# Performance work log

Hardware: AMD Instinct MI355X
Metric: run time of the kernel (lower is better)

The kernel has to match this reference:

```python
import jax, jax.numpy as jnp
import numpy as np

N = 2048
D_T = 256; D_F = 256
E_T = 32; E_F = 32; E_C = 128
C = 5; Q = 512


def setup_inputs() -> dict:
    key = jax.random.key(0)
    ks = jax.random.split(key, 12)
    # full graph minus self-loops, row-major (matches dense_to_sparse ordering)
    r, c = np.meshgrid(np.arange(N), np.arange(N), indexing='ij')
    m = r != c
    edge_index = jnp.asarray(np.stack([r[m], c[m]]), dtype=jnp.int32)  # [2, N*(N-1)]
    E = edge_index.shape[1]
    s = 0.02
    return {
        'time_features': jax.random.normal(ks[0], (N, D_T), jnp.float32),
        'edge_index': edge_index,
        'time_edge_weight': jax.random.uniform(ks[1], (E,), jnp.float32),
        'freq_features': jax.random.normal(ks[2], (N, D_F), jnp.float32),
        'freq_edge_weight': jax.random.uniform(ks[3], (E,), jnp.float32),
        'labels': jax.random.randint(ks[4], (N,), 0, C, jnp.int32),
        'num_classes': C,
        'query_size': Q,
        'Wt': jax.random.normal(ks[5], (D_T, E_T), jnp.float32) * s,
        'bt': jnp.zeros((E_T,), jnp.float32),
        'Wf': jax.random.normal(ks[6], (D_F, E_F), jnp.float32) * s,
        'bf': jnp.zeros((E_F,), jnp.float32),
        'Wc': jax.random.normal(ks[7], (E_T + E_F + C, E_C), jnp.float32) * s,
        'bc': jnp.zeros((E_C,), jnp.float32),
        'Wo': jax.random.normal(ks[8], (E_C, C), jnp.float32) * s,
        'bo': jnp.zeros((C,), jnp.float32),
    }


def _gcn(x, A, W, b):
    # torch_geometric GCNConv: D^{-1/2}(A + I)D^{-1/2} (X W) + b
    n = A.shape[0]
    Ah = A + jnp.eye(n, dtype=A.dtype)
    deg = Ah.sum(axis=1)
    dis = jnp.where(deg > 0, jax.lax.rsqrt(deg), 0.0)
    return (dis[:, None] * Ah * dis[None, :]) @ (x @ W) + b


def reference(time_features, edge_index, time_edge_weight, freq_features,
              freq_edge_weight, labels, num_classes, query_size,
              Wt, bt, Wf, bf, Wc, bc, Wo, bo):
    n = time_features.shape[0]
    lrelu = lambda z: jax.nn.leaky_relu(z, 0.01)

    def dense_adj(w):  # A[dst, src] = w
        return jnp.zeros((n, n), w.dtype).at[edge_index[1], edge_index[0]].add(w)

    te = lrelu(_gcn(time_features, dense_adj(time_edge_weight), Wt, bt))
    fe = lrelu(_gcn(freq_features, dense_adj(freq_edge_weight), Wf, bf))

    # to_one_hot: one_hot[:n - query_size, labels] = 1 -> support rows get 1 in
    # every column that appears anywhere in `labels`
    cols = jnp.zeros((num_classes,), te.dtype).at[labels].set(1.0)
    rowmask = (jnp.arange(n) < (n - query_size)).astype(te.dtype)
    one_hot = rowmask[:, None] * cols[None, :]

    feats = jnp.concatenate([te, fe, one_hot], axis=-1)  # [n, E_T+E_F+C]

    # graph_construction (no_grad in original): 1 / (L1 distance over the
    # non-one-hot dims + 1e-5), zero diagonal
    fd = jax.lax.stop_gradient(feats[:, : feats.shape[1] - num_classes])
    dist = jnp.sum(jnp.abs(fd[:, None, :] - fd[None, :, :]), axis=-1)  # [n, n]
    Aw = (1.0 / (dist + 1e-5)) * (1.0 - jnp.eye(n, dtype=feats.dtype))

    emb = lrelu(_gcn(feats, Aw, Wc, bc))
    return emb @ Wo + bo
```

## Files before the change

### kernel.cpp

```cpp
#include <hip/hip_runtime.h>
#include <hip/hip_bf16.h>

#define N 2048
#define NM1 2047
#define DT 256
#define ET 32
#define EC 128
#define NC 5
#define FS 80
#define FD 69
#define KC_ET 16
#define KC_EC 16

typedef unsigned short u16;
typedef float f32x4 __attribute__((ext_vector_type(4)));
typedef __bf16 bf16x8 __attribute__((ext_vector_type(8)));

__device__ inline u16 bf16_rne(float x){
    unsigned int b = __float_as_uint(x);
    b += 0x7fffu + ((b >> 16) & 1u);
    return (u16)(b >> 16);
}
__device__ inline float bf16_to_f(u16 h){
    return __uint_as_float(((unsigned int)h) << 16);
}
__device__ inline f32x4 mfma16x16x32(bf16x8 a, bf16x8 b, f32x4 c){
    return __builtin_amdgcn_mfma_f32_16x16x32_bf16(a, b, c, 0, 0, 0);
}

__global__ __launch_bounds__(256) void k_deg_label_xw(const float* __restrict__ tw,
                                                      const float* __restrict__ fw,
                                                      const int* __restrict__ labels,
                                                      const float* __restrict__ Xt,
                                                      const float* __restrict__ Wt,
                                                      const float* __restrict__ Xf,
                                                      const float* __restrict__ Wf,
                                                      float* __restrict__ degT,
                                                      float* __restrict__ degF,
                                                      float* __restrict__ cols,
                                                      float* __restrict__ Yt,
                                                      float* __restrict__ Yf){
    int b = blockIdx.x;
    int t = threadIdx.x;
    if (b < 512){
        int p = (b & 7)*256 + t;
        if (p >= NM1) return;
        int s0 = (b >> 3)*32;
        float lowT=0.f, highT=0.f, lowF=0.f, highF=0.f;
        #pragma unroll 8
        for (int r = 0; r < 32; ++r){
            int s = s0 + r;
            float vt = tw[(size_t)s*NM1 + p];
            float vf = fw[(size_t)s*NM1 + p];
            if (s <= p){ highT += vt; highF += vf; }
            else       { lowT  += vt; lowF  += vf; }
        }
        atomicAdd(&degT[p],   lowT);
        atomicAdd(&degF[p],   lowF);
        atomicAdd(&degT[p+1], highT);
        atomicAdd(&degF[p+1], highF);
        return;
    }
    if (b == 512){
        __shared__ float lc[NC];
        if (t < NC) lc[t] = 0.f;
        __syncthreads();
        for (int i = t; i < N; i += 256){
            int l = labels[i];
            if (l >= 0 && l < NC) lc[l] = 1.f;
        }
        __syncthreads();
        if (t < NC) cols[t] = lc[t];
        return;
    }
    int idx = b - 513;
    const float* X = (idx & 256) ? Xf : Xt;
    const float* W = (idx & 256) ? Wf : Wt;
    float*       Y = (idx & 256) ? Yf : Yt;
    __shared__ float Ws[DT*ET];
    __shared__ float Xs[8*DT];
    for (int j = t; j < DT*ET; j += 256) Ws[j] = W[j];
    int i0 = (idx & 255)*8;
    for (int j = t; j < 8*DT; j += 256) Xs[j] = X[(size_t)i0*DT + j];
    __syncthreads();
    int r = t >> 5, f = t & 31;
    const float* xr = Xs + r*DT;
    float acc = 0.f;
    #pragma unroll 8
    for (int d = 0; d < DT; ++d) acc += xr[d]*Ws[d*ET+f];
    Y[(size_t)(i0+r)*ET+f] = acc;
}

__global__ __launch_bounds__(256) void k_agg_et_m(const float* __restrict__ tw,
                                                  const float* __restrict__ fw,
                                                  const float* __restrict__ Yt,
                                                  const float* __restrict__ Yf,
                                                  const float* __restrict__ degT,
                                                  const float* __restrict__ degF,
                                                  float* __restrict__ Pt,
                                                  float* __restrict__ Pf){
    __shared__ u16 Zs[2][2][32][136];
    int t = threadIdx.x;
    int w = t >> 6, l = t & 63, lr = l & 15, lg = l >> 4;
    int g = w >> 1, wh = w & 1;
    int i0 = blockIdx.x*64;
    int kc = blockIdx.y;
    int k0 = kc*128;

    {
        int f = t >> 3;
        int kb16 = (t & 7)*16;
        #pragma unroll
        for (int gg = 0; gg < 2; ++gg){
            const float* Y   = gg ? Yf   : Yt;
            const float* deg = gg ? degF : degT;
            u16 h8[16], l8[16];
            #pragma unroll
            for (int j = 0; j < 16; ++j){
                int k = k0 + kb16 + j;
                float rd = rsqrtf(1.f + deg[k]);
                float v = rd * Y[(size_t)k*ET + f];
                u16 h = bf16_rne(v);
                h8[j] = h;
                l8[j] = bf16_rne(v - bf16_to_f(h));
            }
            uint4 pk;
            pk.x = (unsigned)h8[0] | ((unsigned)h8[1]<<16);
            pk.y = (unsigned)h8[2] | ((unsigned)h8[3]<<16);
            pk.z = (unsigned)h8[4] | ((unsigned)h8[5]<<16);
            pk.w = (unsigned)h8[6] | ((unsigned)h8[7]<<16);
            *(uint4*)&Zs[gg][0][f][kb16] = pk;
            pk.x = (unsigned)h8[8] | ((unsigned)h8[9]<<16);
            pk.y = (unsigned)h8[10] | ((unsigned)h8[11]<<16);
            pk.z = (unsigned)h8[12] | ((unsigned)h8[13]<<16);
            pk.w = (unsigned)h8[14] | ((unsigned)h8[15]<<16);
            *(uint4*)&Zs[gg][0][f][kb16+8] = pk;
            pk.x = (unsigned)l8[0] | ((unsigned)l8[1]<<16);
            pk.y = (unsigned)l8[2] | ((unsigned)l8[3]<<16);
            pk.z = (unsigned)l8[4] | ((unsigned)l8[5]<<16);
            pk.w = (unsigned)l8[6] | ((unsigned)l8[7]<<16);
            *(uint4*)&Zs[gg][1][f][kb16] = pk;
            pk.x = (unsigned)l8[8] | ((unsigned)l8[9]<<16);
            pk.y = (unsigned)l8[10] | ((unsigned)l8[11]<<16);
            pk.z = (unsigned)l8[12] | ((unsigned)l8[13]<<16);
            pk.w = (unsigned)l8[14] | ((unsigned)l8[15]<<16);
            *(uint4*)&Zs[gg][1][f][kb16+8] = pk;
        }
    }
    __syncthreads();

    const float* A = g ? fw : tw;
    f32x4 acc[2][2];
    #pragma unroll
    for (int fi = 0; fi < 2; ++fi)
        #pragma unroll
        for (int ff = 0; ff < 2; ++ff) acc[fi][ff] = (f32x4){0.f,0.f,0.f,0.f};

    for (int sub = 0; sub < 2; ++sub){
        int kb = k0 + sub*64;
        #pragma unroll
        for (int fi = 0; fi < 2; ++fi){
            int row = i0 + wh*32 + fi*16 + lr;
            #pragma unroll
            for (int ks = 0; ks < 2; ++ks){
                int kbase = kb + ks*32 + lg*8;
                u16 ah[8], al[8];
                #pragma unroll
                for (int j = 0; j < 8; ++j){
                    int k = kbase + j;
                    float v = 0.f;
                    if (row != k) v = A[(size_t)k*NM1 + row - (row > k ? 1 : 0)];
                    u16 h = bf16_rne(v);
                    ah[j] = h;
                    al[j] = bf16_rne(v - bf16_to_f(h));
                }
                uint4 pa, pb;
                pa.x = (unsigned)ah[0] | ((unsigned)ah[1]<<16);
                pa.y = (unsigned)ah[2] | ((unsigned)ah[3]<<16);
                pa.z = (unsigned)ah[4] | ((unsigned)ah[5]<<16);
                pa.w = (unsigned)ah[6] | ((unsigned)ah[7]<<16);
                pb.x = (unsigned)al[0] | ((unsigned)al[1]<<16);
                pb.y = (unsigned)al[2] | ((unsigned)al[3]<<16);
                pb.z = (unsigned)al[4] | ((unsigned)al[5]<<16);
                pb.w = (unsigned)al[6] | ((unsigned)al[7]<<16);
                bf16x8 aH = *(bf16x8*)&pa;
                bf16x8 aL = *(bf16x8*)&pb;
                int koff = sub*64 + ks*32 + lg*8;
                #pragma unroll
                for (int ff = 0; ff < 2; ++ff){
                    bf16x8 bH = *(const bf16x8*)&Zs[g][0][ff*16+lr][koff];
                    bf16x8 bL = *(const bf16x8*)&Zs[g][1][ff*16+lr][koff];
                    acc[fi][ff] = mfma16x16x32(aH, bH, acc[fi][ff]);
                    acc[fi][ff] = mfma16x16x32(aL, bH, acc[fi][ff]);
                    acc[fi][ff] = mfma16x16x32(aH, bL, acc[fi][ff]);
                }
            }
        }
    }
    float* P = g ? Pf : Pt;
    #pragma unroll
    for (int fi = 0; fi < 2; ++fi)
        #pragma unroll
        for (int ff = 0; ff < 2; ++ff)
            #pragma unroll
            for (int r = 0; r < 4; ++r){
                int gi = i0 + wh*32 + fi*16 + lg*4 + r;
                P[(size_t)kc*(N*ET) + (size_t)gi*ET + ff*16 + lr] = acc[fi][ff][r];
            }
}

__global__ __launch_bounds__(256) void k_feats_epi(const float* __restrict__ Pt,
                                                   const float* __restrict__ Pf,
                                                   const float* __restrict__ Yt,
                                                   const float* __restrict__ Yf,
                                                   const float* __restrict__ degT,
                                                   const float* __restrict__ degF,
                                                   const float* __restrict__ bt,
                                                   const float* __restrict__ bfv,
                                                   const float* __restrict__ cols,
                                                   const int* __restrict__ qsize,
                                                   float* __restrict__ feats){
    int idx = blockIdx.x*256 + threadIdx.x;
    int i = idx >> 6;
    int f = idx & 63;
    float s, rd, b;
    if (f < ET){
        rd = rsqrtf(1.f + degT[i]);
        s = rd*Yt[(size_t)i*ET + f];
        #pragma unroll
        for (int kc = 0; kc < KC_ET; ++kc) s += Pt[(size_t)kc*(N*ET) + (size_t)i*ET + f];
        b = bt[f];
    } else {
        int g = f - ET;
        rd = rsqrtf(1.f + degF[i]);
        s = rd*Yf[(size_t)i*ET + g];
        #pragma unroll
        for (int kc = 0; kc < KC_ET; ++kc) s += Pf[(size_t)kc*(N*ET) + (size_t)i*ET + g];
        b = bfv[g];
    }
    float v = rd*s + b;
    feats[(size_t)i*FS + f] = v > 0.f ? v : 0.01f*v;
    if (f < NC){
        int nsup = N - qsize[0];
        feats[(size_t)i*FS + 2*ET + f] = (i < nsup) ? cols[f] : 0.f;
    }
}

__global__ __launch_bounds__(256) void k_aw_zc(const float* __restrict__ feats,
                                               const float* __restrict__ Wc,
                                               u16* __restrict__ Aw_hi,
                                               u16* __restrict__ Aw_lo,
                                               u16* __restrict__ ZcT_hi,
                                               u16* __restrict__ ZcT_lo,
                                               float* __restrict__ dsum){
    __shared__ __align__(16) char sm[37632];
    int t = threadIdx.x;
    int b = blockIdx.x;
    if (b < 1024){
        float* fiT = (float*)sm;
        float* fjT = fiT + 64*68;
        int i0 = (b & 31)*64, j0 = (b >> 5)*64;
        {
            int row = t >> 2;
            int cb  = (t & 3)*16;
            const float4* si = (const float4*)(feats + (size_t)(i0+row)*FS + cb);
            const float4* sj = (const float4*)(feats + (size_t)(j0+row)*FS + cb);
            #pragma unroll
            for (int s = 0; s < 4; ++s){
                float4 v = si[s];
                float4 w = sj[s];
                int c = cb + s*4;
                fiT[(c+0)*68+row]=v.x; fiT[(c+1)*68+row]=v.y; fiT[(c+2)*68+row]=v.z; fiT[(c+3)*68+row]=v.w;
                fjT[(c+0)*68+row]=w.x; fjT[(c+1)*68+row]=w.y; fjT[(c+2)*68+row]=w.z; fjT[(c+3)*68+row]=w.w;
            }
        }
        __syncthreads();
        int tx = t & 15, ty = t >> 4;
        float acc[4][4];
        #pragma unroll
        for (int u=0;u<4;++u)
            #pragma unroll
            for (int v=0;v<4;++v) acc[u][v]=0.f;
        for (int d = 0; d < 64; ++d){
            float4 a4 = *(const float4*)&fiT[d*68 + ty*4];
            float4 b4 = *(const float4*)&fjT[d*68 + tx*4];
            const float* ap = (const float*)&a4;
            const float* bp = (const float*)&b4;
            #pragma unroll
            for (int u = 0; u < 4; ++u)
                #pragma unroll
                for (int v = 0; v < 4; ++v)
                    acc[u][v] += fabsf(ap[u]-bp[v]);
        }
        #pragma unroll
        for (int u = 0; u < 4; ++u){
            int gi = i0 + ty*4 + u;
            float po[4];
            u16 hh[4], ll[4];
            #pragma unroll
            for (int v = 0; v < 4; ++v){
                int gj = j0 + tx*4 + v;
                float w = (gi==gj) ? 1.0f : 1.0f/(acc[u][v] + 1e-5f);
                po[v] = w;
                u16 h = bf16_rne(w);
                hh[v] = h;
                ll[v] = bf16_rne(w - bf16_to_f(h));
            }
            uint2 ph, pl;
            ph.x = (unsigned)hh[0] | ((unsigned)hh[1]<<16);
            ph.y = (unsigned)hh[2] | ((unsigned)hh[3]<<16);
            pl.x = (unsigned)ll[0] | ((unsigned)ll[1]<<16);
            pl.y = (unsigned)ll[2] | ((unsigned)ll[3]<<16);
            *(uint2*)&Aw_hi[(size_t)gi*N + j0 + tx*4] = ph;
            *(uint2*)&Aw_lo[(size_t)gi*N + j0 + tx*4] = pl;
            float rs = (po[0]+po[1]) + (po[2]+po[3]);
            rs += __shfl_xor(rs, 1);
            rs += __shfl_xor(rs, 2);
            rs += __shfl_xor(rs, 4);
            rs += __shfl_xor(rs, 8);
            if (tx == 0) atomicAdd(&dsum[gi], rs);
        }
        return;
    }
    {
        float* Wcs = (float*)sm;
        float* fr  = Wcs + FD*EC;
        int idx = b - 1024;
        int i0 = idx*8;
        for (int j = t; j < FD*EC; j += 256) Wcs[j] = Wc[j];
        for (int j = t; j < 8*FD; j += 256){
            int r = j / FD;
            int c = j - r*FD;
            fr[r*72 + c] = feats[(size_t)(i0+r)*FS + c];
        }
        __syncthreads();
        int f  = t & 127;
        int rh = t >> 7;
        u16 hh[4], ll[4];
        #pragma unroll
        for (int rr = 0; rr < 4; ++rr){
            int r = rh*4 + rr;
            float acc = 0.f;
            #pragma unroll
            for (int d = 0; d < FD; ++d) acc += fr[r*72+d]*Wcs[d*EC+f];
            u16 h = bf16_rne(acc);
            hh[rr] = h;
            ll[rr] = bf16_rne(acc - bf16_to_f(h));
        }
        uint2 ph, pl;
        ph.x = (unsigned)hh[0] | ((unsigned)hh[1]<<16);
        ph.y = (unsigned)hh[2] | ((unsigned)hh[3]<<16);
        pl.x = (unsigned)ll[0] | ((unsigned)ll[1]<<16);
        pl.y = (unsigned)ll[2] | ((unsigned)ll[3]<<16);
        *(uint2*)&ZcT_hi[(size_t)f*N + i0 + rh*4] = ph;
        *(uint2*)&ZcT_lo[(size_t)f*N + i0 + rh*4] = pl;
    }
}

__global__ __launch_bounds__(256) void k_agg_ec(const u16* __restrict__ Aw_hi,
                                                const u16* __restrict__ Aw_lo,
                                                const u16* __restrict__ ZcT_hi,
                                                const u16* __restrict__ ZcT_lo,
                                                const float* __restrict__ dsum,
                                                float* __restrict__ Pe){
    __shared__ u16 Ah[64*72];
    __shared__ u16 Al[64*72];
    __shared__ u16 Zh[128*72];
    __shared__ u16 Zl[128*72];
    int t = threadIdx.x;
    int w  = t >> 6;
    int l  = t & 63;
    int lr = l & 15;
    int lg = l >> 4;
    int i0 = blockIdx.x*64;
    int kb0 = blockIdx.y*128;
    f32x4 acc[8];
    #pragma unroll
    for (int tt = 0; tt < 8; ++tt) acc[tt] = (f32x4){0.f, 0.f, 0.f, 0.f};

    for (int sub = 0; sub < 2; ++sub){
        int kbs = kb0 + sub*64;
        #pragma unroll
        for (int e = 0; e < 2; ++e){
            int id = t + e*256;
            int row = id >> 3, ch = (id & 7)*8;
            uint4 vh = *(const uint4*)&Aw_hi[(size_t)(i0+row)*N + kbs + ch];
            uint4 vl = *(const uint4*)&Aw_lo[(size_t)(i0+row)*N + kbs + ch];
            const u16* ph = (const u16*)&vh;
            const u16* pl = (const u16*)&vl;
            u16 nh[8], nl[8];
            #pragma unroll
            for (int j = 0; j < 8; ++j){
                float a = bf16_to_f(ph[j]) + bf16_to_f(pl[j]);
                float v = a * rsqrtf(dsum[kbs + ch + j]);
                u16 h = bf16_rne(v);
                nh[j] = h;
                nl[j] = bf16_rne(v - bf16_to_f(h));
            }
            uint4 oh, ol;
            oh.x = (unsigned)nh[0] | ((unsigned)nh[1]<<16);
            oh.y = (unsigned)nh[2] | ((unsigned)nh[3]<<16);
            oh.z = (unsigned)nh[4] | ((unsigned)nh[5]<<16);
            oh.w = (unsigned)nh[6] | ((unsigned)nh[7]<<16);
            ol.x = (unsigned)nl[0] | ((unsigned)nl[1]<<16);
            ol.y = (unsigned)nl[2] | ((unsigned)nl[3]<<16);
            ol.z = (unsigned)nl[4] | ((unsigned)nl[5]<<16);
            ol.w = (unsigned)nl[6] | ((unsigned)nl[7]<<16);
            *(uint4*)&Ah[row*72 + ch] = oh;
            *(uint4*)&Al[row*72 + ch] = ol;
        }
        #pragma unroll
        for (int e = 0; e < 4; ++e){
            int id = t + e*256;
            int row = id >> 3, ch = (id & 7)*8;
            uint4 vh = *(const uint4*)&ZcT_hi[(size_t)row*N + kbs + ch];
            uint4 vl = *(const uint4*)&ZcT_lo[(size_t)row*N + kbs + ch];
            *(uint4*)&Zh[row*72 + ch] = vh;
            *(uint4*)&Zl[row*72 + ch] = vl;
        }
        __syncthreads();
        #pragma unroll
        for (int ks = 0; ks < 2; ++ks){
            int aoff = (w*16 + lr)*72 + ks*32 + lg*8;
            bf16x8 aH = *(const bf16x8*)&Ah[aoff];
            bf16x8 aL = *(const bf16x8*)&Al[aoff];
            #pragma unroll
            for (int tt = 0; tt < 8; ++tt){
                int zoff = (tt*16 + lr)*72 + ks*32 + lg*8;
                bf16x8 bH = *(const bf16x8*)&Zh[zoff];
                bf16x8 bL = *(const bf16x8*)&Zl[zoff];
                acc[tt] = mfma16x16x32(aH, bH, acc[tt]);
                acc[tt] = mfma16x16x32(aL, bH, acc[tt]);
                acc[tt] = mfma16x16x32(aH, bL, acc[tt]);
            }
        }
        __syncthreads();
    }
    #pragma unroll
    for (int tt = 0; tt < 8; ++tt){
        #pragma unroll
        for (int r = 0; r < 4; ++r){
            int gi = i0 + w*16 + lg*4 + r;
            Pe[(size_t)blockIdx.y*(N*EC) + (size_t)gi*EC + tt*16 + lr] = acc[tt][r];
        }
    }
}

__global__ __launch_bounds__(256) void k_embfinal(const float* __restrict__ Pe,
                                                  const float* __restrict__ dsum,
                                                  const float* __restrict__ bc,
                                                  const float* __restrict__ Wo,
                                                  const float* __restrict__ bo,
                                                  float* __restrict__ out){
    __shared__ float vs[2][EC];
    __shared__ float Wos[EC*NC];
    __shared__ float bos[NC];
    int t = threadIdx.x;
    for (int idx = t; idx < EC*NC; idx += 256) Wos[idx] = Wo[idx];
    if (t < NC) bos[t] = bo[t];
    int rr = t >> 7, f = t & 127;
    int i = blockIdx.x*2 + rr;
    size_t idx = (size_t)i*EC + f;
    float s = 0.f;
    #pragma unroll
    for (int kc = 0; kc < KC_EC; ++kc) s += Pe[(size_t)kc*(N*EC) + idx];
    float v = rsqrtf(dsum[i])*s + bc[f];
    vs[rr][f] = v > 0.f ? v : 0.01f*v;
    __syncthreads();
    if (t < 2*NC){
        int r = t / NC;
        int c = t - r*NC;
        float a = bos[c];
        #pragma unroll 8
        for (int f2 = 0; f2 < EC; ++f2) a += vs[r][f2]*Wos[f2*NC+c];
        out[(size_t)(blockIdx.x*2 + r)*NC + c] = a;
    }
}

extern "C" void kernel_launch(void* const* d_in, const int* in_sizes, int n_in,
                              void* d_out, int out_size, void* d_ws, size_t ws_size,
                              hipStream_t stream) {
    const float* time_features = (const float*)d_in[0];
    const float* tw            = (const float*)d_in[2];
    const float* freq_features = (const float*)d_in[3];
    const float* fw            = (const float*)d_in[4];
    const int*   labels        = (const int*)d_in[5];
    const int*   qsize         = (const int*)d_in[7];
    const float* Wt  = (const float*)d_in[8];
    const float* bt  = (const float*)d_in[9];
    const float* Wf  = (const float*)d_in[10];
    const float* bfv = (const float*)d_in[11];
    const float* Wc  = (const float*)d_in[12];
    const float* bc  = (const float*)d_in[13];
    const float* Wo  = (const float*)d_in[14];
    const float* bo  = (const float*)d_in[15];
    float* out = (float*)d_out;

    float* ws    = (float*)d_ws;
    float* degT  = ws;
    float* degF  = degT + N;
    float* dsum  = degF + N;
    float* colsb = dsum + N;
    float* Yt    = colsb + 8;
    float* Yf    = Yt + (size_t)N*ET;
    float* feats = Yf + (size_t)N*ET;
    float* Zc    = feats + (size_t)N*FS;
    float* Aw    = Zc + (size_t)N*EC;
    float* Pt    = Aw + (size_t)N*N;
    float* Pf    = Pt + (size_t)KC_ET*N*ET;
    float* Pe    = Pf + (size_t)KC_ET*N*ET;

    u16* ZcT_hi = (u16*)Zc;
    u16* ZcT_lo = ZcT_hi + (size_t)N*EC;
    u16* Aw_hi  = (u16*)Aw;
    u16* Aw_lo  = Aw_hi + (size_t)N*N;

    hipMemsetAsync(degT, 0, 3*N*sizeof(float), stream);
    k_deg_label_xw<<<1025, 256, 0, stream>>>(tw, fw, labels,
                                             time_features, Wt, freq_features, Wf,
                                             degT, degF, colsb, Yt, Yf);
    k_agg_et_m<<<dim3(N/64, KC_ET), 256, 0, stream>>>(tw, fw, Yt, Yf, degT, degF, Pt, Pf);
    k_feats_epi<<<(N*64)/256, 256, 0, stream>>>(Pt, Pf, Yt, Yf, degT, degF,
                                                bt, bfv, colsb, qsize, feats);
    k_aw_zc<<<1280, 256, 0, stream>>>(feats, Wc, Aw_hi, Aw_lo, ZcT_hi, ZcT_lo, dsum);
    k_agg_ec<<<dim3(N/64, KC_EC), 256, 0, stream>>>(Aw_hi, Aw_lo, ZcT_hi, ZcT_lo, dsum, Pe);
    k_embfinal<<<N/2, 256, 0, stream>>>(Pe, dsum, bc, Wo, bo, out);
}
```

Measured before the change: 191.1 us.

## Stage edge-weight tiles through LDS with coalesced loads in time/freq aggregation

The first-layer aggregation kernel now loads the edge-weight block cooperatively into shared memory. Consecutive threads read consecutive destination rows, so the gathers from the row-major edge list are coalesced, whereas before each lane gathered strided elements directly into MFMA fragments. Each block now handles both graphs one after the other with all four waves on one graph, instead of splitting waves between the time and frequency graphs. This adds extra barriers and LDS traffic in exchange for better global-memory access patterns.

```diff
diff --git a/kernel.cpp b/kernel.cpp
--- a/kernel.cpp
+++ b/kernel.cpp
@@ -13,6 +13,7 @@
 #define KC_EC 16
 
 typedef unsigned short u16;
+typedef unsigned int u32;
 typedef float f32x4 __attribute__((ext_vector_type(4)));
 typedef __bf16 bf16x8 __attribute__((ext_vector_type(8)));
 
@@ -91,29 +92,32 @@
     Y[(size_t)(i0+r)*ET+f] = acc;
 }
 
-__global__ __launch_bounds__(256) void k_agg_et_m(const float* __restrict__ tw,
-                                                  const float* __restrict__ fw,
-                                                  const float* __restrict__ Yt,
-                                                  const float* __restrict__ Yf,
-                                                  const float* __restrict__ degT,
-                                                  const float* __restrict__ degF,
-                                                  float* __restrict__ Pt,
-                                                  float* __restrict__ Pf){
-    __shared__ u16 Zs[2][2][32][136];
+__global__ __launch_bounds__(256) void k_agg_et_m2(const float* __restrict__ tw,
+                                                   const float* __restrict__ fw,
+                                                   const float* __restrict__ Yt,
+                                                   const float* __restrict__ Yf,
+                                                   const float* __restrict__ degT,
+                                                   const float* __restrict__ degF,
+                                                   float* __restrict__ Pt,
+                                                   float* __restrict__ Pf){
+    __shared__ u16 Zs[2][32][136];
+    __shared__ u16 As[2][64][72];
     int t = threadIdx.x;
     int w = t >> 6, l = t & 63, lr = l & 15, lg = l >> 4;
-    int g = w >> 1, wh = w & 1;
     int i0 = blockIdx.x*64;
     int kc = blockIdx.y;
     int k0 = kc*128;
 
-    {
-        int f = t >> 3;
-        int kb16 = (t & 7)*16;
-        #pragma unroll
-        for (int gg = 0; gg < 2; ++gg){
-            const float* Y   = gg ? Yf   : Yt;
-            const float* deg = gg ? degF : degT;
+    for (int g = 0; g < 2; ++g){
+        const float* A   = g ? fw   : tw;
+        const float* Y   = g ? Yf   : Yt;
+        const float* deg = g ? degF : degT;
+        float*       P   = g ? Pf   : Pt;
+
+        __syncthreads();
+        {
+            int f = t >> 3;
+            int kb16 = (t & 7)*16;
             u16 h8[16], l8[16];
             #pragma unroll
             for (int j = 0; j < 16; ++j){
@@ -125,88 +129,75 @@
                 l8[j] = bf16_rne(v - bf16_to_f(h));
             }
             uint4 pk;
-            pk.x = (unsigned)h8[0] | ((unsigned)h8[1]<<16);
-            pk.y = (unsigned)h8[2] | ((unsigned)h8[3]<<16);
-            pk.z = (unsigned)h8[4] | ((unsigned)h8[5]<<16);
-            pk.w = (unsigned)h8[6] | ((unsigned)h8[7]<<16);
-            *(uint4*)&Zs[gg][0][f][kb16] = pk;
-            pk.x = (unsigned)h8[8] | ((unsigned)h8[9]<<16);
-            pk.y = (unsigned)h8[10] | ((unsigned)h8[11]<<16);
-            pk.z = (unsigned)h8[12] | ((unsigned)h8[13]<<16);
-            pk.w = (unsigned)h8[14] | ((unsigned)h8[15]<<16);
-            *(uint4*)&Zs[gg][0][f][kb16+8] = pk;
-            pk.x = (unsigned)l8[0] | ((unsigned)l8[1]<<16);
-            pk.y = (unsigned)l8[2] | ((unsigned)l8[3]<<16);
-            pk.z = (unsigned)l8[4] | ((unsigned)l8[5]<<16);
-            pk.w = (unsigned)l8[6] | ((unsigned)l8[7]<<16);
-            *(uint4*)&Zs[gg][1][f][kb16] = pk;
-            pk.x = (unsigned)l8[8] | ((unsigned)l8[9]<<16);
-            pk.y = (unsigned)l8[10] | ((unsigned)l8[11]<<16);
-            pk.z = (unsigned)l8[12] | ((unsigned)l8[13]<<16);
-            pk.w = (unsigned)l8[14] | ((unsigned)l8[15]<<16);
-            *(uint4*)&Zs[gg][1][f][kb16+8] = pk;
-        }
-    }
-    __syncthreads();
-
-    const float* A = g ? fw : tw;
-    f32x4 acc[2][2];
-    #pragma unroll
-    for (int fi = 0; fi < 2; ++fi)
-        #pragma unroll
-        for (int ff = 0; ff < 2; ++ff) acc[fi][ff] = (f32x4){0.f,0.f,0.f,0.f};
-
-    for (int sub = 0; sub < 2; ++sub){
-        int kb = k0 + sub*64;
-        #pragma unroll
-        for (int fi = 0; fi < 2; ++fi){
-            int row = i0 + wh*32 + fi*16 + lr;
+            pk.x = (u32)h8[0] | ((u32)h8[1]<<16);
+            pk.y = (u32)h8[2] | ((u32)h8[3]<<16);
+            pk.z = (u32)h8[4] | ((u32)h8[5]<<16);
+            pk.w = (u32)h8[6] | ((u32)h8[7]<<16);
+            *(uint4*)&Zs[0][f][kb16] = pk;
+            pk.x = (u32)h8[8]  | ((u32)h8[9]<<16);
+            pk.y = (u32)h8[10] | ((u32)h8[11]<<16);
+            pk.z = (u32)h8[12] | ((u32)h8[13]<<16);
+            pk.w = (u32)h8[14] | ((u32)h8[15]<<16);
+            *(uint4*)&Zs[0][f][kb16+8] = pk;
+            pk.x = (u32)l8[0] | ((u32)l8[1]<<16);
+            pk.y = (u32)l8[2] | ((u32)l8[3]<<16);
+            pk.z = (u32)l8[4] | ((u32)l8[5]<<16);
+            pk.w = (u32)l8[6] | ((u32)l8[7]<<16);
+            *(uint4*)&Zs[1][f][kb16] = pk;
+            pk.x = (u32)l8[8]  | ((u32)l8[9]<<16);
+            pk.y = (u32)l8[10] | ((u32)l8[11]<<16);
+            pk.z = (u32)l8[12] | ((u32)l8[13]<<16);
+            pk.w = (u32)l8[14] | ((u32)l8[15]<<16);
+            *(uint4*)&Zs[1][f][kb16+8] = pk;
+        }
+
+        f32x4 acc[2];
+        acc[0] = (f32x4){0.f,0.f,0.f,0.f};
+        acc[1] = (f32x4){0.f,0.f,0.f,0.f};
+
+        for (int sub = 0; sub < 2; ++sub){
+            int kbs = k0 + sub*64;
+            __syncthreads();
+            #pragma unroll
+            for (int e = 0; e < 8; ++e){
+                int id = t + e*256;
+                int kp  = id >> 6;
+                int i_l = id & 63;
+                int k  = kbs + kp*2;
+                int gi = i0 + i_l;
+                float v0 = 0.f, v1 = 0.f;
+                if (gi != k)   v0 = A[(size_t)k*NM1 + gi - (gi > k ? 1 : 0)];
+                if (gi != k+1) v1 = A[(size_t)(k+1)*NM1 + gi - (gi > k+1 ? 1 : 0)];
+                u16 h0 = bf16_rne(v0);
+                u16 l0 = bf16_rne(v0 - bf16_to_f(h0));
+                u16 h1 = bf16_rne(v1);
+                u16 l1 = bf16_rne(v1 - bf16_to_f(h1));
+                *(u32*)&As[0][i_l][kp*2] = (u32)h0 | ((u32)h1<<16);
+                *(u32*)&As[1][i_l][kp*2] = (u32)l0 | ((u32)l1<<16);
+            }
+            __syncthreads();
             #pragma unroll
             for (int ks = 0; ks < 2; ++ks){
-                int kbase = kb + ks*32 + lg*8;
-                u16 ah[8], al[8];
+                bf16x8 aH = *(const bf16x8*)&As[0][w*16 + lr][ks*32 + lg*8];
+                bf16x8 aL = *(const bf16x8*)&As[1][w*16 + lr][ks*32 + lg*8];
                 #pragma unroll
-                for (int j = 0; j < 8; ++j){
-                    int k = kbase + j;
-                    float v = 0.f;
-                    if (row != k) v = A[(size_t)k*NM1 + row - (row > k ? 1 : 0)];
-                    u16 h = bf16_rne(v);
-                    ah[j] = h;
-                    al[j] = bf16_rne(v - bf16_to_f(h));
+                for (int cf = 0; cf < 2; ++cf){
+                    bf16x8 bH = *(const bf16x8*)&Zs[0][cf*16 + lr][sub*64 + ks*32 + lg*8];
+                    bf16x8 bL = *(const bf16x8*)&Zs[1][cf*16 + lr][sub*64 + ks*32 + lg*8];
+                    acc[cf] = mfma16x16x32(aH, bH, acc[cf]);
+                    acc[cf] = mfma16x16x32(aL, bH, acc[cf]);
+                    acc[cf] = mfma16x16x32(aH, bL, acc[cf]);
                 }
-                uint4 pa, pb;
-                pa.x = (unsigned)ah[0] | ((unsigned)ah[1]<<16);
-                pa.y = (unsigned)ah[2] | ((unsigned)ah[3]<<16);
-                pa.z = (unsigned)ah[4] | ((unsigned)ah[5]<<16);
-                pa.w = (unsigned)ah[6] | ((unsigned)ah[7]<<16);
-                pb.x = (unsigned)al[0] | ((unsigned)al[1]<<16);
-                pb.y = (unsigned)al[2] | ((unsigned)al[3]<<16);
-                pb.z = (unsigned)al[4] | ((unsigned)al[5]<<16);
-                pb.w = (unsigned)al[6] | ((unsigned)al[7]<<16);
-                bf16x8 aH = *(bf16x8*)&pa;
-                bf16x8 aL = *(bf16x8*)&pb;
-                int koff = sub*64 + ks*32 + lg*8;
-                #pragma unroll
-                for (int ff = 0; ff < 2; ++ff){
-                    bf16x8 bH = *(const bf16x8*)&Zs[g][0][ff*16+lr][koff];
-                    bf16x8 bL = *(const bf16x8*)&Zs[g][1][ff*16+lr][koff];
-                    acc[fi][ff] = mfma16x16x32(aH, bH, acc[fi][ff]);
-                    acc[fi][ff] = mfma16x16x32(aL, bH, acc[fi][ff]);
-                    acc[fi][ff] = mfma16x16x32(aH, bL, acc[fi][ff]);
-                }
-            }
-        }
-    }
-    float* P = g ? Pf : Pt;
-    #pragma unroll
-    for (int fi = 0; fi < 2; ++fi)
-        #pragma unroll
-        for (int ff = 0; ff < 2; ++ff)
+            }
+        }
+        #pragma unroll
+        for (int cf = 0; cf < 2; ++cf)
             #pragma unroll
             for (int r = 0; r < 4; ++r){
-                int gi = i0 + wh*32 + fi*16 + lg*4 + r;
-                P[(size_t)kc*(N*ET) + (size_t)gi*ET + ff*16 + lr] = acc[fi][ff][r];
-            }
+                int gi = i0 + w*16 + lg*4 + r;
+                P[(size_t)kc*(N*ET) + (size_t)gi*ET + cf*16 + lr] = acc[cf][r];
+            }
+    }
 }
 
 __global__ __launch_bounds__(256) void k_feats_epi(const float* __restrict__ Pt,
@@ -307,10 +298,10 @@
                 ll[v] = bf16_rne(w - bf16_to_f(h));
             }
             uint2 ph, pl;
-            ph.x = (unsigned)hh[0] | ((unsigned)hh[1]<<16);
-            ph.y = (unsigned)hh[2] | ((unsigned)hh[3]<<16);
-            pl.x = (unsigned)ll[0] | ((unsigned)ll[1]<<16);
-            pl.y = (unsigned)ll[2] | ((unsigned)ll[3]<<16);
+            ph.x = (u32)hh[0] | ((u32)hh[1]<<16);
+            ph.y = (u32)hh[2] | ((u32)hh[3]<<16);
+            pl.x = (u32)ll[0] | ((u32)ll[1]<<16);
+            pl.y = (u32)ll[2] | ((u32)ll[3]<<16);
             *(uint2*)&Aw_hi[(size_t)gi*N + j0 + tx*4] = ph;
             *(uint2*)&Aw_lo[(size_t)gi*N + j0 + tx*4] = pl;
             float rs = (po[0]+po[1]) + (po[2]+po[3]);
@@ -348,10 +339,10 @@
             ll[rr] = bf16_rne(acc - bf16_to_f(h));
         }
         uint2 ph, pl;
-        ph.x = (unsigned)hh[0] | ((unsigned)hh[1]<<16);
-        ph.y = (unsigned)hh[2] | ((unsigned)hh[3]<<16);
-        pl.x = (unsigned)ll[0] | ((unsigned)ll[1]<<16);
-        pl.y = (unsigned)ll[2] | ((unsigned)ll[3]<<16);
+        ph.x = (u32)hh[0] | ((u32)hh[1]<<16);
+        ph.y = (u32)hh[2] | ((u32)hh[3]<<16);
+        pl.x = (u32)ll[0] | ((u32)ll[1]<<16);
+        pl.y = (u32)ll[2] | ((u32)ll[3]<<16);
         *(uint2*)&ZcT_hi[(size_t)f*N + i0 + rh*4] = ph;
         *(uint2*)&ZcT_lo[(size_t)f*N + i0 + rh*4] = pl;
     }
@@ -398,14 +389,14 @@
                 nl[j] = bf16_rne(v - bf16_to_f(h));
             }
             uint4 oh, ol;
-            oh.x = (unsigned)nh[0] | ((unsigned)nh[1]<<16);
-            oh.y = (unsigned)nh[2] | ((unsigned)nh[3]<<16);
-            oh.z = (unsigned)nh[4] | ((unsigned)nh[5]<<16);
-            oh.w = (unsigned)nh[6] | ((unsigned)nh[7]<<16);
-            ol.x = (unsigned)nl[0] | ((unsigned)nl[1]<<16);
-            ol.y = (unsigned)nl[2] | ((unsigned)nl[3]<<16);
-            ol.z = (unsigned)nl[4] | ((unsigned)nl[5]<<16);
-            ol.w = (unsigned)nl[6] | ((unsigned)nl[7]<<16);
+            oh.x = (u32)nh[0] | ((u32)nh[1]<<16);
+            oh.y = (u32)nh[2] | ((u32)nh[3]<<16);
+            oh.z = (u32)nh[4] | ((u32)nh[5]<<16);
+            oh.w = (u32)nh[6] | ((u32)nh[7]<<16);
+            ol.x = (u32)nl[0] | ((u32)nl[1]<<16);
+            ol.y = (u32)nl[2] | ((u32)nl[3]<<16);
+            ol.z = (u32)nl[4] | ((u32)nl[5]<<16);
+            ol.w = (u32)nl[6] | ((u32)nl[7]<<16);
             *(uint4*)&Ah[row*72 + ch] = oh;
             *(uint4*)&Al[row*72 + ch] = ol;
         }
@@ -519,7 +510,7 @@
     k_deg_label_xw<<<1025, 256, 0, stream>>>(tw, fw, labels,
                                              time_features, Wt, freq_features, Wf,
                                              degT, degF, colsb, Yt, Yf);
-    k_agg_et_m<<<dim3(N/64, KC_ET), 256, 0, stream>>>(tw, fw, Yt, Yf, degT, degF, Pt, Pf);
+    k_agg_et_m2<<<dim3(N/64, KC_ET), 256, 0, stream>>>(tw, fw, Yt, Yf, degT, degF, Pt, Pf);
     k_feats_epi<<<(N*64)/256, 256, 0, stream>>>(Pt, Pf, Yt, Yf, degT, degF,
                                                 bt, bfv, colsb, qsize, feats);
     k_aw_zc<<<1280, 256, 0, stream>>>(feats, Wc, Aw_hi, Aw_lo, ZcT_hi, ZcT_lo, dsum);
```

Measured after the change: 197.2 us. 1.03x slower.
